# Kernel optimization log

Hardware: AMD Instinct MI355X
Metric: run time of the kernel (lower is better)

The kernel has to match this reference:

```python
import jax, jax.numpy as jnp
import numpy as np

N = 8192
E = 262144
IN_DIM = 128
OUT_DIM = 16


def _linear_params(key, fan_in, fan_out):
    k1, k2 = jax.random.split(key)
    bound = 1.0 / np.sqrt(fan_in)
    W = jax.random.uniform(k1, (fan_in, fan_out), jnp.float32, -bound, bound)
    b = jax.random.uniform(k2, (fan_out,), jnp.float32, -bound, bound)
    return W, b


def setup_inputs() -> dict:
    key = jax.random.key(0)
    ks = jax.random.split(key, 10)
    x = jax.random.normal(ks[0], (N, IN_DIM), jnp.float32)
    edge_index = jax.random.randint(ks[1], (2, E), 0, N, jnp.int64)
    W1, b1 = _linear_params(ks[2], IN_DIM, 128)
    W2, b2 = _linear_params(ks[3], 128, 256)
    W3, b3 = _linear_params(ks[4], 256, 64)
    Wk, bk = _linear_params(ks[5], 256, 256)
    Wq, bq = _linear_params(ks[6], 256, 256)
    Wr, br = _linear_params(ks[7], IN_DIM, 64)
    Wf, bf = _linear_params(ks[8], 64, OUT_DIM)
    ln_g = jnp.ones((64,), jnp.float32)
    ln_b = jnp.zeros((64,), jnp.float32)
    return dict(x=x, edge_index=edge_index, W1=W1, b1=b1, W2=W2, b2=b2,
                W3=W3, b3=b3, Wk=Wk, bk=bk, Wq=Wq, bq=bq, Wr=Wr, br=br,
                ln_g=ln_g, ln_b=ln_b, Wf=Wf, bf=bf)


def gcn_conv(x, W, b, row, col, n):
    # PyG GCNConv: add self-loops, symmetric normalization, aggregate src->dst
    xw = x @ W                                          # [N, F_out]
    loops = jnp.arange(n, dtype=row.dtype)
    r = jnp.concatenate([row, loops])
    c = jnp.concatenate([col, loops])
    deg = jax.ops.segment_sum(jnp.ones_like(c, jnp.float32), c, num_segments=n)
    dinv = jnp.where(deg > 0, jax.lax.rsqrt(jnp.maximum(deg, 1e-12)), 0.0)
    norm = dinv[r] * dinv[c]                            # [E+N]
    out = jax.ops.segment_sum(norm[:, None] * xw[r], c, num_segments=n)
    return out + b


def _forward(x, edge_index, W1, b1, W2, b2, W3, b3, Wk, bk, Wq, bq,
             Wr, br, ln_g, ln_b, Wf, bf):
    row, col = edge_index[0], edge_index[1]
    n = x.shape[0]
    residual = x @ Wr + br                              # [N, 64]
    h = jax.nn.leaky_relu(gcn_conv(x, W1, b1, row, col, n))   # dropout = eval no-op
    h = jax.nn.leaky_relu(gcn_conv(h, W2, b2, row, col, n))   # [N, 256]
    keys = h @ Wk + bk
    queries = h @ Wq + bq
    scores = queries @ keys.T                           # [N, N] dense, as in source
    mask = jnp.zeros((n, n), jnp.float32).at[row, col].set(1.0)
    scores = scores * mask                              # multiplicative mask (faithful)
    attn = jax.nn.softmax(scores, axis=-1)
    h = attn @ h                                        # [N, 256]
    h = jax.nn.leaky_relu(gcn_conv(h, W3, b3, row, col, n))   # [N, 64]
    z = h + residual
    mu = jnp.mean(z, axis=-1, keepdims=True)
    var = jnp.mean((z - mu) ** 2, axis=-1, keepdims=True)
    z = (z - mu) * jax.lax.rsqrt(var + 1e-5) * ln_g + ln_b
    pooled = jnp.max(z, axis=0)                         # 'max' pooling -> [64]
    return pooled @ Wf + bf                             # [OUT_DIM]


def reference(x, edge_index, W1, b1, W2, b2, W3, b3, Wk, bk, Wq, bq,
              Wr, br, ln_g, ln_b, Wf, bf):
    return _forward(x, edge_index, W1, b1, W2, b2, W3, b3, Wk, bk, Wq, bq,
                    Wr, br, ln_g, ln_b, Wf, bf)
```

## Files before the change

### kernel.cpp

```cpp
#include <hip/hip_runtime.h>
#include <hip/hip_fp16.h>
#include <cstdint>
#include <cstddef>

#define NNODES 8192
#define NEDGES 262144
#define MAXDEG 96
#define SMEM_BYTES 10496

typedef _Float16 f16x8 __attribute__((ext_vector_type(8)));
typedef _Float16 h2v   __attribute__((ext_vector_type(2)));
typedef float    f32x4 __attribute__((ext_vector_type(4)));

__device__ __forceinline__ float leaky(float v){ return v > 0.f ? v : 0.01f*v; }

__device__ __forceinline__ unsigned fmap(float f){
  unsigned u = __float_as_uint(f);
  return (u & 0x80000000u) ? ~u : (u | 0x80000000u);
}
__device__ __forceinline__ float funmap(unsigned u){
  return (u & 0x80000000u) ? __uint_as_float(u & 0x7FFFFFFFu) : __uint_as_float(~u);
}
__device__ __forceinline__ h2v as_h2(unsigned u){
  union{ unsigned x; h2v h; } c; c.x = u; return c.h;
}

struct GP {
  const float *x; const int *ei;
  const float *W1,*b1,*W2,*b2,*W3,*b3,*Wk,*bk,*Wq,*bq,*Wr,*br,*lng,*lnb,*Wf,*bfv;
  float* out;
  __half *xh,*xw1h,*h1h,*h1ah,*h2h,*qth,*gh,*hw3h;
  float *resid,*sw3;
  __half *Wqh,*Wkh,*Wqkt,*Wrt,*W1t,*W2t,*W3t;
  float *bqk,*wb,*s0p;
  int *degc,*degr,*csrc,*csrd;
  unsigned* poolpart;
};

__device__ __forceinline__ void pre_unit(const GP& p, int b, char* smem){
  int t = threadIdx.x;
  if (b < 1024){
    int base = (b*256 + t)*4;
    float4 xv = *(const float4*)(p.x + base);
    uint2 o;
    *(__half2*)&o.x = __floats2half2_rn(xv.x, xv.y);
    *(__half2*)&o.y = __floats2half2_rn(xv.z, xv.w);
    *(uint2*)(p.xh + base) = o;
  } else if (b < 1088){
    int base = ((b-1024)*256 + t)*4;
    float4 v = *(const float4*)(p.Wq + base);
    uint2 o;
    *(__half2*)&o.x = __floats2half2_rn(v.x, v.y);
    *(__half2*)&o.y = __floats2half2_rn(v.z, v.w);
    *(uint2*)(p.Wqh + base) = o;
  } else if (b < 1152){
    int base = ((b-1088)*256 + t)*4;
    float4 v = *(const float4*)(p.Wk + base);
    uint2 o;
    *(__half2*)&o.x = __floats2half2_rn(v.x, v.y);
    *(__half2*)&o.y = __floats2half2_rn(v.z, v.w);
    *(uint2*)(p.Wkh + base) = o;
  } else if (b < 1184){
    int idx = (b-1152)*256 + t;
    int nn = idx >> 7, k = idx & 127;
    p.Wrt[idx] = __float2half(p.Wr[k*64 + nn]);
  } else if (b < 1248){
    int idx = (b-1184)*256 + t;
    int nn = idx >> 7, k = idx & 127;
    p.W1t[idx] = __float2half(p.W1[k*128 + nn]);
  } else if (b < 1376){
    int idx = (b-1248)*256 + t;
    int nn = idx >> 7, k = idx & 127;
    p.W2t[idx] = __float2half(p.W2[k*256 + nn]);
  } else if (b < 1440){
    int idx = (b-1376)*256 + t;
    int nn = idx >> 8, k = idx & 255;
    p.W3t[idx] = __float2half(p.W3[k*64 + nn]);
  } else if (b < 1504){
    int idx = (b-1440)*256 + t;
    if (idx < 8192) p.degc[idx]=0; else p.degr[idx-8192]=0;
  } else if (b < 1520){
    p.poolpart[(b-1504)*256 + t] = 0u;
  } else if (b == 1520){
    if (t < 64) p.sw3[t]=0.f;
  } else {
    int c = b - 1521;
    float* ra = (float*)smem; float* rb = ra + 256; float* rc = rb + 256;
    ra[t] = p.Wk[c*256 + t] * p.bq[t];
    rb[t] = p.Wq[c*256 + t] * p.bk[t];
    if (c == 0) rc[t] = p.bq[t]*p.bk[t];
    __syncthreads();
    for (int off=128; off; off>>=1){
      if (t < off){
        ra[t] += ra[t+off];
        rb[t] += rb[t+off];
        if (c == 0) rc[t] += rc[t+off];
      }
      __syncthreads();
    }
    if (t == 0){
      p.bqk[c] = ra[0];
      p.wb[c]  = rb[0];
      if (c == 0) p.s0p[0] = rc[0];
    }
  }
}

__device__ __forceinline__ void gemm_tile(const __half* __restrict__ A,
    const __half* __restrict__ Bt, const float* __restrict__ bias,
    float* __restrict__ Cf, __half* __restrict__ Ch, float* __restrict__ csum,
    int K, int N, int act, int bx, int by,
    _Float16 (*As)[40], _Float16 (*Bs)[40], float* cs){
  int t = threadIdx.x, w = t>>6, lane = t&63;
  int m0 = bx*64, n0 = by*64;
  int quad = lane>>4, l15 = lane&15;
  int srow = t>>2, soff = (t&3)*8;
  f32x4 acc0 = {0.f,0.f,0.f,0.f}, acc1 = acc0, acc2 = acc0, acc3 = acc0;
  for (int k0 = 0; k0 < K; k0 += 32){
    *(uint4*)&As[srow][soff] = *(const uint4*)(A  + (size_t)(m0+srow)*K + k0 + soff);
    *(uint4*)&Bs[srow][soff] = *(const uint4*)(Bt + (size_t)(n0+srow)*K + k0 + soff);
    __syncthreads();
    f16x8 af = *(const f16x8*)&As[w*16 + l15][quad*8];
    f16x8 b0 = *(const f16x8*)&Bs[ 0 + l15][quad*8];
    f16x8 b1 = *(const f16x8*)&Bs[16 + l15][quad*8];
    f16x8 b2 = *(const f16x8*)&Bs[32 + l15][quad*8];
    f16x8 b3 = *(const f16x8*)&Bs[48 + l15][quad*8];
    acc0 = __builtin_amdgcn_mfma_f32_16x16x32_f16(af, b0, acc0, 0,0,0);
    acc1 = __builtin_amdgcn_mfma_f32_16x16x32_f16(af, b1, acc1, 0,0,0);
    acc2 = __builtin_amdgcn_mfma_f32_16x16x32_f16(af, b2, acc2, 0,0,0);
    acc3 = __builtin_amdgcn_mfma_f32_16x16x32_f16(af, b3, acc3, 0,0,0);
    __syncthreads();
  }
  f32x4 accs[4] = {acc0, acc1, acc2, acc3};
  if (csum){
    if (t < 64) cs[t] = 0.f;
    __syncthreads();
    #pragma unroll
    for (int nt=0; nt<4; ++nt){
      float pp = accs[nt][0]+accs[nt][1]+accs[nt][2]+accs[nt][3];
      atomicAdd(&cs[nt*16 + l15], pp);
    }
    __syncthreads();
    if (t < 64) atomicAdd(&csum[n0 + t], cs[t]);
  }
  #pragma unroll
  for (int nt=0; nt<4; ++nt){
    int col = n0 + nt*16 + l15;
    float bv = bias ? bias[col] : 0.f;
    #pragma unroll
    for (int r=0;r<4;r++){
      int row = m0 + w*16 + quad*4 + r;
      float v = accs[nt][r] + bv;
      if (act) v = leaky(v);
      if (Cf) Cf[(size_t)row*N + col] = v;
      if (Ch) Ch[(size_t)row*N + col] = __float2half(v);
    }
  }
}

__device__ __forceinline__ void agg128_unit(const __half* __restrict__ in,
    const int* __restrict__ deg, const int* __restrict__ src,
    __half* __restrict__ outp,
    const float* __restrict__ bias, int act, int c, char* smem){
  int t = threadIdx.x, w = t>>6, lane = t&63;
  int dcc = deg[c];
  float dc = rsqrtf((float)(dcc+1));
  float2 acc = make_float2(0.f, 0.f);
  int e0 = c*MAXDEG, e1 = e0 + dcc;
  for (int eb = e0 + w*4; eb < e1; eb += 16){
    int m = e1 - eb; if (m > 4) m = 4;
    int r[4];
    #pragma unroll
    for (int u=0;u<4;u++) r[u] = src[(u<m) ? eb+u : eb];
    float sc[4]; __half2 hv[4];
    #pragma unroll
    for (int u=0;u<4;u++){
      sc[u] = rsqrtf((float)(deg[r[u]]+1));
      hv[u] = *(const __half2*)(in + (size_t)r[u]*128 + lane*2);
    }
    #pragma unroll
    for (int u=0;u<4;u++){
      if (u < m){
        float2 h = __half22float2(hv[u]);
        acc.x = fmaf(sc[u], h.x, acc.x);
        acc.y = fmaf(sc[u], h.y, acc.y);
      }
    }
  }
  float2 (*red)[64] = (float2(*)[64])smem;
  red[w][lane] = acc;
  __syncthreads();
  if (w == 0){
    float2 s = red[0][lane];
    float2 b1 = red[1][lane], b2 = red[2][lane], b3 = red[3][lane];
    s.x += b1.x + b2.x + b3.x;
    s.y += b1.y + b2.y + b3.y;
    float2 self = __half22float2(*(const __half2*)(in + (size_t)c*128 + lane*2));
    float ox = dc*(dc*self.x + s.x);
    float oy = dc*(dc*self.y + s.y);
    if (act){
      ox = leaky(ox + bias[lane*2]);
      oy = leaky(oy + bias[lane*2+1]);
    }
    *(__half2*)(outp + (size_t)c*128 + lane*2) = __floats2half2_rn(ox, oy);
  }
}

__device__ __forceinline__ void attn_unit(const GP& p, int u){
  const int n = NNODES;
  int w = threadIdx.x>>6, lane = threadIdx.x&63;
  int i = u*4 + w;
  int fo = lane*4;
  uint2 qtu = *(const uint2*)(p.qth + (size_t)i*256 + fo);
  h2v q0 = as_h2(qtu.x), q1 = as_h2(qtu.y);
  float4 wbv = *(const float4*)(p.wb + fo);
  uint2 hiu  = *(const uint2*)(p.h2h + (size_t)i*256 + fo);
  float2 hia = __half22float2(*(__half2*)&hiu.x);
  float2 hib = __half22float2(*(__half2*)&hiu.y);
  float pv = hia.x*wbv.x + hia.y*wbv.y + hib.x*wbv.z + hib.y*wbv.w;
  #pragma unroll
  for (int mm=32; mm; mm>>=1) pv += __shfl_xor(pv, mm, 64);
  float Ei = __expf(pv + p.s0p[0]);
  int dri = p.degr[i];
  int e0 = i*MAXDEG, e1 = e0 + dri;
  float acc = 0.f, dsum = 0.f;
  for (int eb = e0; eb < e1; eb += 8){
    int m = e1 - eb; if (m > 8) m = 8;
    int j[8];
    #pragma unroll
    for (int u8=0;u8<8;u8++) j[u8] = p.csrd[(u8<m) ? eb+u8 : eb];
    uint2 hv[8]; float gv[8];
    #pragma unroll
    for (int u8=0;u8<8;u8++){
      hv[u8] = *(const uint2*)(p.h2h + (size_t)j[u8]*256 + fo);
      gv[u8] = __half2float(p.gh[(size_t)j[u8]*64 + lane]);
    }
    float d[8];
    #pragma unroll
    for (int u8=0;u8<8;u8++)
      d[u8] = __builtin_amdgcn_fdot2(q1, as_h2(hv[u8].y),
              __builtin_amdgcn_fdot2(q0, as_h2(hv[u8].x), 0.f, false), false);
    #pragma unroll
    for (int mm=32; mm; mm>>=1){
      #pragma unroll
      for (int u8=0;u8<8;u8++) d[u8] += __shfl_xor(d[u8], mm, 64);
    }
    #pragma unroll
    for (int u8=0;u8<8;u8++){
      if (u8 < m){
        float we = Ei * __expf(d[u8]);
        dsum += we;
        acc = fmaf(we - 1.f, gv[u8], acc);
      }
    }
  }
  float inv = 1.0f / ((float)(n - dri) + dsum);
  p.hw3h[(size_t)i*64 + lane] = __float2half((p.sw3[lane] + acc) * inv);
}

__device__ __forceinline__ void zp_unit(const GP& p, int c, char* smem){
  int t = threadIdx.x, w = t>>6, lane = t&63;
  int dcc = p.degc[c];
  float dc = rsqrtf((float)(dcc+1));
  float acc = 0.f;
  int e0 = c*MAXDEG, e1 = e0 + dcc;
  for (int eb = e0 + w*4; eb < e1; eb += 16){
    int m = e1 - eb; if (m > 4) m = 4;
    int r[4];
    #pragma unroll
    for (int u=0;u<4;u++) r[u] = p.csrc[(u<m) ? eb+u : eb];
    float sc[4]; __half hval[4];
    #pragma unroll
    for (int u=0;u<4;u++){
      sc[u] = rsqrtf((float)(p.degc[r[u]]+1));
      hval[u] = p.hw3h[(size_t)r[u]*64 + lane];
    }
    #pragma unroll
    for (int u=0;u<4;u++)
      if (u < m) acc = fmaf(sc[u], __half2float(hval[u]), acc);
  }
  float (*red)[64] = (float(*)[64])smem;
  red[w][lane] = acc;
  __syncthreads();
  if (w == 0){
    acc = red[0][lane]+red[1][lane]+red[2][lane]+red[3][lane];
    float self = __half2float(p.hw3h[(size_t)c*64 + lane]);
    float v = leaky(dc*(dc*self + acc) + p.b3[lane]) + p.resid[(size_t)c*64 + lane];
    float s = v;
    #pragma unroll
    for (int mm=32; mm; mm>>=1) s += __shfl_xor(s, mm, 64);
    float mu = s * (1.0f/64.0f);
    float d = v - mu;
    float s2 = d*d;
    #pragma unroll
    for (int mm=32; mm; mm>>=1) s2 += __shfl_xor(s2, mm, 64);
    float zv = d * rsqrtf(s2*(1.0f/64.0f) + 1e-5f) * p.lng[lane] + p.lnb[lane];
    atomicMax(&p.poolpart[(c & 63)*64 + lane], fmap(zv));
  }
}

__device__ __forceinline__ void final_unit(const GP& p, char* smem){
  int t = threadIdx.x, f = t & 63, g = t >> 6;
  unsigned (*sm)[64] = (unsigned(*)[64])smem;
  float* pool = (float*)(smem + 1024);
  unsigned mu = 0u;
  for (int b = g; b < 64; b += 4) mu = max(mu, p.poolpart[b*64 + f]);
  sm[g][f] = mu;
  __syncthreads();
  if (g == 0)
    pool[f] = funmap(max(max(sm[0][f],sm[1][f]), max(sm[2][f],sm[3][f])));
  __syncthreads();
  if (t < 16){
    float a = p.bfv[t];
    #pragma unroll
    for (int ff=0; ff<64; ++ff) a = fmaf(pool[ff], p.Wf[ff*16 + t], a);
    p.out[t] = a;
  }
}

__global__ __launch_bounds__(256) void k_pre(GP p){
  __shared__ __align__(16) char smem[SMEM_BYTES];
  pre_unit(p, blockIdx.x, smem);
}

__global__ __launch_bounds__(256) void k_sc(GP p){
  __shared__ __align__(16) char smem[SMEM_BYTES];
  _Float16 (*As)[40] = (_Float16(*)[40])smem;
  _Float16 (*Bs)[40] = (_Float16(*)[40])(smem + 5120);
  int b = blockIdx.x;
  if (b < 1024){
    int e = b*256 + threadIdx.x;
    int r = p.ei[e], c = p.ei[NEDGES+e];
    int p1 = atomicAdd(&p.degc[c],1); p.csrc[c*MAXDEG + p1] = r;
    int p2 = atomicAdd(&p.degr[r],1); p.csrd[r*MAXDEG + p2] = c;
  } else if (b < 1280){
    int bb = b - 1024;
    gemm_tile(p.xh, p.W1t, nullptr, nullptr, p.xw1h, nullptr, 128, 128, 0, bb>>1, bb&1, As, Bs, nullptr);
  } else if (b < 1296){
    int bb = b - 1280;
    gemm_tile(p.Wkh, p.Wqh, nullptr, nullptr, p.Wqkt, nullptr, 256, 256, 0, bb&3, bb>>2, As, Bs, nullptr);
  } else {
    gemm_tile(p.xh, p.Wrt, p.br, p.resid, nullptr, nullptr, 128, 64, 0, b-1296, 0, As, Bs, nullptr);
  }
}

__global__ __launch_bounds__(256) void k_agg(GP p, int which){
  __shared__ __align__(16) char smem[SMEM_BYTES];
  if (which == 0)
    agg128_unit(p.xw1h, p.degc, p.csrc, p.h1h, p.b1, 1, blockIdx.x, smem);
  else
    agg128_unit(p.h1h, p.degc, p.csrc, p.h1ah, nullptr, 0, blockIdx.x, smem);
}

__global__ __launch_bounds__(256) void k_gemm2(GP p){
  __shared__ __align__(16) char smem[SMEM_BYTES];
  _Float16 (*As)[40] = (_Float16(*)[40])smem;
  _Float16 (*Bs)[40] = (_Float16(*)[40])(smem + 5120);
  int b = blockIdx.x;
  gemm_tile(p.h1ah, p.W2t, p.b2, nullptr, p.h2h, nullptr, 128, 256, 1, b>>2, b&3, As, Bs, nullptr);
}

__global__ __launch_bounds__(256) void k_mix2(GP p){
  __shared__ __align__(16) char smem[SMEM_BYTES];
  _Float16 (*As)[40] = (_Float16(*)[40])smem;
  _Float16 (*Bs)[40] = (_Float16(*)[40])(smem + 5120);
  float* cs = (float*)(smem + 10240);
  int b = blockIdx.x;
  if (b < 128) gemm_tile(p.h2h, p.W3t, nullptr, nullptr, p.gh, p.sw3, 256, 64, 0, b, 0, As, Bs, cs);
  else {
    int bb = b - 128;
    gemm_tile(p.h2h, p.Wqkt, p.bqk, nullptr, p.qth, nullptr, 256, 256, 0, bb>>2, bb&3, As, Bs, cs);
  }
}

__global__ __launch_bounds__(256) void k_attn(GP p){ attn_unit(p, blockIdx.x); }

__global__ __launch_bounds__(256) void k_zp(GP p){
  __shared__ __align__(16) char smem[SMEM_BYTES];
  zp_unit(p, blockIdx.x, smem);
}

__global__ __launch_bounds__(256) void k_final(GP p){
  __shared__ __align__(16) char smem[SMEM_BYTES];
  final_unit(p, smem);
}

extern "C" void kernel_launch(void* const* d_in, const int* in_sizes, int n_in,
                              void* d_out, int out_size, void* d_ws, size_t ws_size,
                              hipStream_t stream){
  const int n = NNODES, E = NEDGES;
  char* ws = (char*)d_ws; size_t off = 0;
  auto alloc = [&](size_t bytes)->void*{
    void* pp = ws + off; off += (bytes + 255) & ~(size_t)255; return pp;
  };
  GP p;
  p.x   = (const float*)d_in[0];
  p.ei  = (const int*)d_in[1];
  p.W1  = (const float*)d_in[2];  p.b1 = (const float*)d_in[3];
  p.W2  = (const float*)d_in[4];  p.b2 = (const float*)d_in[5];
  p.W3  = (const float*)d_in[6];  p.b3 = (const float*)d_in[7];
  p.Wk  = (const float*)d_in[8];  p.bk = (const float*)d_in[9];
  p.Wq  = (const float*)d_in[10]; p.bq = (const float*)d_in[11];
  p.Wr  = (const float*)d_in[12]; p.br = (const float*)d_in[13];
  p.lng = (const float*)d_in[14]; p.lnb = (const float*)d_in[15];
  p.Wf  = (const float*)d_in[16]; p.bfv = (const float*)d_in[17];
  p.out = (float*)d_out;

  p.xh   = (__half*)alloc((size_t)n*128*2);
  p.xw1h = (__half*)alloc((size_t)n*128*2);
  p.h1h  = (__half*)alloc((size_t)n*128*2);
  p.h1ah = (__half*)alloc((size_t)n*128*2);
  p.h2h  = (__half*)alloc((size_t)n*256*2);
  p.qth  = (__half*)alloc((size_t)n*256*2);
  p.gh   = (__half*)alloc((size_t)n*64*2);
  p.hw3h = (__half*)alloc((size_t)n*64*2);
  p.resid= (float*)alloc((size_t)n*64*4);
  p.sw3  = (float*)alloc(64*4);
  p.Wqh  = (__half*)alloc(256*256*2);
  p.Wkh  = (__half*)alloc(256*256*2);
  p.Wqkt = (__half*)alloc(256*256*2);
  p.Wrt  = (__half*)alloc(128*64*2);
  p.W1t  = (__half*)alloc(128*128*2);
  p.W2t  = (__half*)alloc(128*256*2);
  p.W3t  = (__half*)alloc(256*64*2);
  p.bqk  = (float*)alloc(256*4);
  p.wb   = (float*)alloc(256*4);
  p.s0p  = (float*)alloc(4);
  p.degc = (int*)alloc((size_t)n*4);
  p.degr = (int*)alloc((size_t)n*4);
  p.csrc = (int*)alloc((size_t)n*MAXDEG*4);
  p.csrd = (int*)alloc((size_t)n*MAXDEG*4);
  p.poolpart = (unsigned*)alloc(64*64*4);

  k_pre  <<<dim3(1777), 256, 0, stream>>>(p);
  k_sc   <<<dim3(1424), 256, 0, stream>>>(p);
  k_agg  <<<dim3(n),    256, 0, stream>>>(p, 0);
  k_agg  <<<dim3(n),    256, 0, stream>>>(p, 1);
  k_gemm2<<<dim3(512),  256, 0, stream>>>(p);
  k_mix2 <<<dim3(640),  256, 0, stream>>>(p);
  k_attn <<<dim3(n/4),  256, 0, stream>>>(p);
  k_zp   <<<dim3(n),    256, 0, stream>>>(p);
  k_final<<<dim3(1),    256, 0, stream>>>(p);
}
```

Measured before the change: 224.4 us.

## Use one wave per node for aggregation and pre-scale by source degree

```diff
diff --git a/kernel.cpp b/kernel.cpp
--- a/kernel.cpp
+++ b/kernel.cpp
@@ -158,52 +158,45 @@
   }
 }
 
-__device__ __forceinline__ void agg128_unit(const __half* __restrict__ in,
+template<int INS, int OUTS, int ACT>
+__device__ __forceinline__ void agg128w(const __half* __restrict__ in,
     const int* __restrict__ deg, const int* __restrict__ src,
-    __half* __restrict__ outp,
-    const float* __restrict__ bias, int act, int c, char* smem){
-  int t = threadIdx.x, w = t>>6, lane = t&63;
-  int dcc = deg[c];
+    __half* __restrict__ outp, const float* __restrict__ bias, int i){
+  int lane = threadIdx.x & 63;
+  int dcc = deg[i];
   float dc = rsqrtf((float)(dcc+1));
+  int e0 = i*MAXDEG, e1 = e0 + dcc;
   float2 acc = make_float2(0.f, 0.f);
-  int e0 = c*MAXDEG, e1 = e0 + dcc;
-  for (int eb = e0 + w*4; eb < e1; eb += 16){
-    int m = e1 - eb; if (m > 4) m = 4;
-    int r[4];
-    #pragma unroll
-    for (int u=0;u<4;u++) r[u] = src[(u<m) ? eb+u : eb];
-    float sc[4]; __half2 hv[4];
-    #pragma unroll
-    for (int u=0;u<4;u++){
-      sc[u] = rsqrtf((float)(deg[r[u]]+1));
+  for (int eb = e0; eb < e1; eb += 8){
+    int m = e1 - eb; if (m > 8) m = 8;
+    int r[8];
+    #pragma unroll
+    for (int u=0;u<8;u++) r[u] = src[(u<m) ? eb+u : eb];
+    __half2 hv[8]; float sc[8];
+    #pragma unroll
+    for (int u=0;u<8;u++){
       hv[u] = *(const __half2*)(in + (size_t)r[u]*128 + lane*2);
-    }
-    #pragma unroll
-    for (int u=0;u<4;u++){
+      sc[u] = INS ? 1.f : rsqrtf((float)(deg[r[u]]+1));
+    }
+    #pragma unroll
+    for (int u=0;u<8;u++){
       if (u < m){
         float2 h = __half22float2(hv[u]);
-        acc.x = fmaf(sc[u], h.x, acc.x);
-        acc.y = fmaf(sc[u], h.y, acc.y);
+        if (INS){ acc.x += h.x; acc.y += h.y; }
+        else { acc.x = fmaf(sc[u], h.x, acc.x); acc.y = fmaf(sc[u], h.y, acc.y); }
       }
     }
   }
-  float2 (*red)[64] = (float2(*)[64])smem;
-  red[w][lane] = acc;
-  __syncthreads();
-  if (w == 0){
-    float2 s = red[0][lane];
-    float2 b1 = red[1][lane], b2 = red[2][lane], b3 = red[3][lane];
-    s.x += b1.x + b2.x + b3.x;
-    s.y += b1.y + b2.y + b3.y;
-    float2 self = __half22float2(*(const __half2*)(in + (size_t)c*128 + lane*2));
-    float ox = dc*(dc*self.x + s.x);
-    float oy = dc*(dc*self.y + s.y);
-    if (act){
-      ox = leaky(ox + bias[lane*2]);
-      oy = leaky(oy + bias[lane*2+1]);
-    }
-    *(__half2*)(outp + (size_t)c*128 + lane*2) = __floats2half2_rn(ox, oy);
-  }
+  float2 self = __half22float2(*(const __half2*)(in + (size_t)i*128 + lane*2));
+  float ss = INS ? 1.f : dc;
+  float ox = dc*(ss*self.x + acc.x);
+  float oy = dc*(ss*self.y + acc.y);
+  if (ACT){
+    ox = leaky(ox + bias[lane*2]);
+    oy = leaky(oy + bias[lane*2+1]);
+  }
+  if (OUTS){ ox *= dc; oy *= dc; }
+  *(__half2*)(outp + (size_t)i*128 + lane*2) = __floats2half2_rn(ox, oy);
 }
 
 __device__ __forceinline__ void attn_unit(const GP& p, int u){
@@ -255,48 +248,40 @@
     }
   }
   float inv = 1.0f / ((float)(n - dri) + dsum);
-  p.hw3h[(size_t)i*64 + lane] = __float2half((p.sw3[lane] + acc) * inv);
-}
-
-__device__ __forceinline__ void zp_unit(const GP& p, int c, char* smem){
-  int t = threadIdx.x, w = t>>6, lane = t&63;
+  float di = rsqrtf((float)(p.degc[i]+1));
+  p.hw3h[(size_t)i*64 + lane] = __float2half(di * (p.sw3[lane] + acc) * inv);
+}
+
+__device__ __forceinline__ void zp_wave(const GP& p, int c){
+  int lane = threadIdx.x & 63;
   int dcc = p.degc[c];
   float dc = rsqrtf((float)(dcc+1));
   float acc = 0.f;
   int e0 = c*MAXDEG, e1 = e0 + dcc;
-  for (int eb = e0 + w*4; eb < e1; eb += 16){
-    int m = e1 - eb; if (m > 4) m = 4;
-    int r[4];
-    #pragma unroll
-    for (int u=0;u<4;u++) r[u] = p.csrc[(u<m) ? eb+u : eb];
-    float sc[4]; __half hval[4];
-    #pragma unroll
-    for (int u=0;u<4;u++){
-      sc[u] = rsqrtf((float)(p.degc[r[u]]+1));
-      hval[u] = p.hw3h[(size_t)r[u]*64 + lane];
-    }
-    #pragma unroll
-    for (int u=0;u<4;u++)
-      if (u < m) acc = fmaf(sc[u], __half2float(hval[u]), acc);
-  }
-  float (*red)[64] = (float(*)[64])smem;
-  red[w][lane] = acc;
-  __syncthreads();
-  if (w == 0){
-    acc = red[0][lane]+red[1][lane]+red[2][lane]+red[3][lane];
-    float self = __half2float(p.hw3h[(size_t)c*64 + lane]);
-    float v = leaky(dc*(dc*self + acc) + p.b3[lane]) + p.resid[(size_t)c*64 + lane];
-    float s = v;
-    #pragma unroll
-    for (int mm=32; mm; mm>>=1) s += __shfl_xor(s, mm, 64);
-    float mu = s * (1.0f/64.0f);
-    float d = v - mu;
-    float s2 = d*d;
-    #pragma unroll
-    for (int mm=32; mm; mm>>=1) s2 += __shfl_xor(s2, mm, 64);
-    float zv = d * rsqrtf(s2*(1.0f/64.0f) + 1e-5f) * p.lng[lane] + p.lnb[lane];
-    atomicMax(&p.poolpart[(c & 63)*64 + lane], fmap(zv));
-  }
+  for (int eb = e0; eb < e1; eb += 8){
+    int m = e1 - eb; if (m > 8) m = 8;
+    int r[8];
+    #pragma unroll
+    for (int u=0;u<8;u++) r[u] = p.csrc[(u<m) ? eb+u : eb];
+    __half hval[8];
+    #pragma unroll
+    for (int u=0;u<8;u++) hval[u] = p.hw3h[(size_t)r[u]*64 + lane];
+    #pragma unroll
+    for (int u=0;u<8;u++)
+      if (u < m) acc += __half2float(hval[u]);
+  }
+  float self = __half2float(p.hw3h[(size_t)c*64 + lane]);
+  float v = leaky(dc*(self + acc) + p.b3[lane]) + p.resid[(size_t)c*64 + lane];
+  float s = v;
+  #pragma unroll
+  for (int mm=32; mm; mm>>=1) s += __shfl_xor(s, mm, 64);
+  float mu = s * (1.0f/64.0f);
+  float d = v - mu;
+  float s2 = d*d;
+  #pragma unroll
+  for (int mm=32; mm; mm>>=1) s2 += __shfl_xor(s2, mm, 64);
+  float zv = d * rsqrtf(s2*(1.0f/64.0f) + 1e-5f) * p.lng[lane] + p.lnb[lane];
+  atomicMax(&p.poolpart[(c & 63)*64 + lane], fmap(zv));
 }
 
 __device__ __forceinline__ void final_unit(const GP& p, char* smem){
@@ -344,12 +329,13 @@
   }
 }
 
-__global__ __launch_bounds__(256) void k_agg(GP p, int which){
-  __shared__ __align__(16) char smem[SMEM_BYTES];
-  if (which == 0)
-    agg128_unit(p.xw1h, p.degc, p.csrc, p.h1h, p.b1, 1, blockIdx.x, smem);
-  else
-    agg128_unit(p.h1h, p.degc, p.csrc, p.h1ah, nullptr, 0, blockIdx.x, smem);
+__global__ __launch_bounds__(256) void k_agg0(GP p){
+  int i = blockIdx.x*4 + (threadIdx.x>>6);
+  agg128w<0,1,1>(p.xw1h, p.degc, p.csrc, p.h1h, p.b1, i);
+}
+__global__ __launch_bounds__(256) void k_agg1(GP p){
+  int i = blockIdx.x*4 + (threadIdx.x>>6);
+  agg128w<1,0,0>(p.h1h, p.degc, p.csrc, p.h1ah, nullptr, i);
 }
 
 __global__ __launch_bounds__(256) void k_gemm2(GP p){
@@ -376,8 +362,8 @@
 __global__ __launch_bounds__(256) void k_attn(GP p){ attn_unit(p, blockIdx.x); }
 
 __global__ __launch_bounds__(256) void k_zp(GP p){
-  __shared__ __align__(16) char smem[SMEM_BYTES];
-  zp_unit(p, blockIdx.x, smem);
+  int c = blockIdx.x*4 + (threadIdx.x>>6);
+  zp_wave(p, c);
 }
 
 __global__ __launch_bounds__(256) void k_final(GP p){
@@ -434,11 +420,11 @@
 
   k_pre  <<<dim3(1777), 256, 0, stream>>>(p);
   k_sc   <<<dim3(1424), 256, 0, stream>>>(p);
-  k_agg  <<<dim3(n),    256, 0, stream>>>(p, 0);
-  k_agg  <<<dim3(n),    256, 0, stream>>>(p, 1);
+  k_agg0 <<<dim3(n/4),  256, 0, stream>>>(p);
+  k_agg1 <<<dim3(n/4),  256, 0, stream>>>(p);
   k_gemm2<<<dim3(512),  256, 0, stream>>>(p);
   k_mix2 <<<dim3(640),  256, 0, stream>>>(p);
   k_attn <<<dim3(n/4),  256, 0, stream>>>(p);
-  k_zp   <<<dim3(n),    256, 0, stream>>>(p);
+  k_zp   <<<dim3(n/4),  256, 0, stream>>>(p);
   k_final<<<dim3(1),    256, 0, stream>>>(p);
 }
```

After: 216.7 us. 1.04x faster.
